# Performance work log

Measured on AMD Instinct MI355X. Metric: run time of the kernel, lower is better.

## Reference

```python
import jax, jax.numpy as jnp
import numpy as np

B, N, D = 4, 8192, 1024
H, DK = 8, 128          # d_k = D // H
FF = 4096
EPS = 1e-5


def setup_inputs() -> dict:
    key = jax.random.key(0)
    ks = jax.random.split(key, 8)
    s = 0.02  # init scale for weights
    return {
        "x": jax.random.normal(ks[0], (B, N, D), jnp.float32),
        "delta_x": jax.random.uniform(ks[1], (N,), jnp.float32),
        # Linear weights stored [in, out] (math-equivalent to torch's x @ W.T)
        "Wq": jax.random.normal(ks[2], (D, D), jnp.float32) * s,
        "bq": jnp.zeros((D,), jnp.float32),
        "Wk": jax.random.normal(ks[3], (D, D), jnp.float32) * s,
        "bk": jnp.zeros((D,), jnp.float32),
        "Wv": jax.random.normal(ks[4], (D, D), jnp.float32) * s,
        "bv": jnp.zeros((D,), jnp.float32),
        # per-head LayerNorm params for K; NOTE: the original code (faithfully
        # reproduced) applies layernorms_K to BOTH key and value in Galerkin mode.
        "gamma_k": jnp.ones((H, DK), jnp.float32),
        "beta_k": jnp.zeros((H, DK), jnp.float32),
        "W1": jax.random.normal(ks[5], (D, FF), jnp.float32) * s,
        "b1": jnp.zeros((FF,), jnp.float32),
        "W2": jax.random.normal(ks[6], (FF, D), jnp.float32) * s,
        "b2": jnp.zeros((D,), jnp.float32),
    }


def _per_head_ln(t, gamma, beta):
    # t: [B, H, N, DK]; torch LayerNorm: biased variance over last dim
    mu = jnp.mean(t, axis=-1, keepdims=True)
    var = jnp.mean(jnp.square(t - mu), axis=-1, keepdims=True)
    t = (t - mu) * jax.lax.rsqrt(var + EPS)
    return t * gamma[None, :, None, :] + beta[None, :, None, :]


def reference(x, delta_x, Wq, bq, Wk, bk, Wv, bv, gamma_k, beta_k, W1, b1, W2, b2):
    b, n, d = x.shape

    def heads(y):  # [b, n, d] -> [b, H, n, DK]
        return y.reshape(b, n, H, DK).transpose(0, 2, 1, 3)

    q = heads(x @ Wq + bq)
    k = heads(x @ Wk + bk)
    v = heads(x @ Wv + bv)

    k = _per_head_ln(k, gamma_k, beta_k)
    v = _per_head_ln(v, gamma_k, beta_k)  # layernorms_K reused on value (as in source)
    k = k * delta_x[None, None, :, None]  # einsum('bhxd,x->bhxd')

    # Galerkin (softmax-free, linear) attention: (K^T V) / N then Q @ (.)
    scores = jnp.einsum("bhnd,bhne->bhde", k, v) / n  # [b,H,DK,DK]
    attn_out = jnp.einsum("bhnd,bhde->bhne", q, scores)  # [b,H,n,DK]
    # (F.dropout in the source treated as identity: inference/eval semantics)

    x = x + attn_out.transpose(0, 2, 1, 3).reshape(b, n, d)  # residual 1
    h = jax.nn.silu(x @ W1 + b1)
    return x + (h @ W2 + b2)  # residual 2
```

## Files before the change

### kernel.cpp

```cpp
#include <hip/hip_runtime.h>
#include <hip/hip_bf16.h>
#include <stdint.h>

#define DEV __device__ __forceinline__

typedef __attribute__((ext_vector_type(8))) short bf16x8;
typedef __attribute__((ext_vector_type(8))) unsigned short u16x8;
typedef __attribute__((ext_vector_type(4))) unsigned short u16x4;
typedef __attribute__((ext_vector_type(4))) float f32x4;

static constexpr int BB = 4, NN = 8192, DD = 1024, HH = 8, DKK = 128, FFF = 4096;
static constexpr int MM = BB * NN;

DEV float bfb2f(unsigned int s) { unsigned int x = s << 16; float f; __builtin_memcpy(&f, &x, 4); return f; }
DEV unsigned short f2bfb(float f) {
    unsigned int x; __builtin_memcpy(&x, &f, 4);
    x += 0x7fffu + ((x >> 16) & 1u);
    return (unsigned short)(x >> 16);
}

DEV void gload_lds16(const void* g, void* l) {
    auto gp = (const __attribute__((address_space(1))) void*)(uintptr_t)g;
    auto lp = (__attribute__((address_space(3))) void*)(unsigned int)(uintptr_t)l;
    __builtin_amdgcn_global_load_lds(gp, lp, 16, 0, 0);
}

__global__ void k_pack_bf16(const float* __restrict__ in, unsigned short* __restrict__ ob, long n) {
    long i = ((long)blockIdx.x * blockDim.x + threadIdx.x) * 8;
    if (i >= n) return;
    f32x4 a = *(const f32x4*)&in[i];
    f32x4 b = *(const f32x4*)&in[i + 4];
    u16x8 o;
    o[0]=f2bfb(a[0]); o[1]=f2bfb(a[1]); o[2]=f2bfb(a[2]); o[3]=f2bfb(a[3]);
    o[4]=f2bfb(b[0]); o[5]=f2bfb(b[1]); o[6]=f2bfb(b[2]); o[7]=f2bfb(b[3]);
    *(u16x8*)&ob[i] = o;
}

__global__ void k_transpose(const float* __restrict__ W, unsigned short* __restrict__ WT, int R, int C) {
    __shared__ float t[32][33];
    const int tid = threadIdx.x;
    const int r0 = blockIdx.y * 32, c0 = blockIdx.x * 32;
    const int lr = tid >> 3, lc = (tid & 7) * 4;
    f32x4 v = *(const f32x4*)&W[(long)(r0 + lr) * C + c0 + lc];
    t[lr][lc + 0] = v[0]; t[lr][lc + 1] = v[1]; t[lr][lc + 2] = v[2]; t[lr][lc + 3] = v[3];
    __syncthreads();
    const int oc = tid >> 3, orr = (tid & 7) * 4;
    u16x4 o;
    o[0] = f2bfb(t[orr + 0][oc]); o[1] = f2bfb(t[orr + 1][oc]);
    o[2] = f2bfb(t[orr + 2][oc]); o[3] = f2bfb(t[orr + 3][oc]);
    *(u16x4*)&WT[(long)(c0 + oc) * R + r0 + orr] = o;
}

template <int EPI>
__global__ __launch_bounds__(512, 2)
void k_gemm256(const unsigned short* __restrict__ A, int lda,
               const unsigned short* __restrict__ BT, int ldbt,
               const float* __restrict__ bias0, const float* __restrict__ bias1,
               const float* __restrict__ bias2,
               const unsigned short* __restrict__ resb,
               unsigned short* __restrict__ outp0, unsigned short* __restrict__ outp1,
               unsigned short* __restrict__ outp2,
               float* __restrict__ outf,
               int K, int gridx)
{
    extern __shared__ __align__(128) unsigned short smem[];
    unsigned short* As = smem;
    unsigned short* Bs = smem + 4 * 8192;

    const int nwg = gridDim.x;
    int wg = blockIdx.x;
    {
        const int q = nwg >> 3, r = nwg & 7;
        const int xcd = wg & 7, idx = wg >> 3;
        wg = (xcd < r ? xcd * (q + 1) : r * (q + 1) + (xcd - r) * q) + idx;
    }
    const int brow = (wg / gridx) * 256;
    const int bcol = (wg % gridx) * 256;

    const int tid = threadIdx.x;
    const int lane = tid & 63;
    const int w = tid >> 6;
    const int wm = w >> 2, wn = w & 3;
    const int fr = lane & 15;
    const int kg = lane >> 4;

    const int dl = tid * 16;
    const int soff = dl ^ (((dl >> 7) & 3) << 4);
    const int arow = soff >> 6;
    const int akel = (soff & 63) >> 1;
    const unsigned short* Abase = A + (long)(brow + arow) * lda + akel;
    const unsigned short* Bbase = BT + (long)(bcol + arow) * ldbt + akel;

#define STAGE2(gb, ldg, slot) do { \
        gload_lds16((gb), (slot) + tid * 8); \
        gload_lds16((gb) + 128 * (long)(ldg), (slot) + 4096 + tid * 8); } while (0)

    auto lds_frag = [&](const unsigned short* slot, int row) -> bf16x8 {
        int off = row * 64 + kg * 16;
        off ^= ((off >> 7) & 3) << 4;
        return *(const bf16x8*)((const char*)slot + off);
    };

    f32x4 acc[8][4] = {};

    STAGE2(Abase, lda, As);
    STAGE2(Bbase, ldbt, Bs);
    STAGE2(Abase + 32, lda, As + 8192);
    STAGE2(Bbase + 32, ldbt, Bs + 8192);
    asm volatile("s_waitcnt vmcnt(4)" ::: "memory");
    __builtin_amdgcn_s_barrier();

    const int NT = K >> 6;
    for (int t = 0; t < NT; ++t) {
        const unsigned short* a0 = As + ((2 * t) & 3) * 8192;
        const unsigned short* a1 = As + ((2 * t + 1) & 3) * 8192;
        const unsigned short* b0 = Bs + ((2 * t) & 3) * 8192;
        const unsigned short* b1 = Bs + ((2 * t + 1) & 3) * 8192;
        unsigned short* nA0 = As + ((2 * t + 2) & 3) * 8192;
        unsigned short* nA1 = As + ((2 * t + 3) & 3) * 8192;
        unsigned short* nB0 = Bs + ((2 * t + 2) & 3) * 8192;
        unsigned short* nB1 = Bs + ((2 * t + 3) & 3) * 8192;
        const bool st = (t + 1 < NT);
        const long kn = (long)(t + 1) * 64;

        bf16x8 b0f[4], a0f[4], a1f[4], b1f[4], a2f[4], a3f[4];
        if (st) STAGE2(Abase + kn, lda, nA0);
        #pragma unroll
        for (int n = 0; n < 4; ++n) b0f[n] = lds_frag(b0, wn * 64 + n * 16 + fr);
        #pragma unroll
        for (int m = 0; m < 4; ++m) a0f[m] = lds_frag(a0, wm * 128 + m * 16 + fr);
        __builtin_amdgcn_s_setprio(1);
        #pragma unroll
        for (int m = 0; m < 4; ++m)
            #pragma unroll
            for (int n = 0; n < 4; ++n)
                acc[m][n] = __builtin_amdgcn_mfma_f32_16x16x32_bf16(a0f[m], b0f[n], acc[m][n], 0, 0, 0);
        __builtin_amdgcn_s_setprio(0);
        __builtin_amdgcn_s_barrier();
        if (st) STAGE2(Bbase + kn, ldbt, nB0);
        #pragma unroll
        for (int m = 0; m < 4; ++m) a1f[m] = lds_frag(a0, wm * 128 + (m + 4) * 16 + fr);
        __builtin_amdgcn_s_setprio(1);
        #pragma unroll
        for (int m = 0; m < 4; ++m)
            #pragma unroll
            for (int n = 0; n < 4; ++n)
                acc[m + 4][n] = __builtin_amdgcn_mfma_f32_16x16x32_bf16(a1f[m], b0f[n], acc[m + 4][n], 0, 0, 0);
        __builtin_amdgcn_s_setprio(0);
        asm volatile("s_waitcnt vmcnt(4)" ::: "memory");
        __builtin_amdgcn_s_barrier();
        if (st) STAGE2(Abase + kn + 32, lda, nA1);
        #pragma unroll
        for (int n = 0; n < 4; ++n) b1f[n] = lds_frag(b1, wn * 64 + n * 16 + fr);
        #pragma unroll
        for (int m = 0; m < 4; ++m) a2f[m] = lds_frag(a1, wm * 128 + m * 16 + fr);
        __builtin_amdgcn_s_setprio(1);
        #pragma unroll
        for (int m = 0; m < 4; ++m)
            #pragma unroll
            for (int n = 0; n < 4; ++n)
                acc[m][n] = __builtin_amdgcn_mfma_f32_16x16x32_bf16(a2f[m], b1f[n], acc[m][n], 0, 0, 0);
        __builtin_amdgcn_s_setprio(0);
        __builtin_amdgcn_s_barrier();
        if (st) STAGE2(Bbase + kn + 32, ldbt, nB1);
        #pragma unroll
        for (int m = 0; m < 4; ++m) a3f[m] = lds_frag(a1, wm * 128 + (m + 4) * 16 + fr);
        __builtin_amdgcn_s_setprio(1);
        #pragma unroll
        for (int m = 0; m < 4; ++m)
            #pragma unroll
            for (int n = 0; n < 4; ++n)
                acc[m + 4][n] = __builtin_amdgcn_mfma_f32_16x16x32_bf16(a3f[m], b1f[n], acc[m + 4][n], 0, 0, 0);
        __builtin_amdgcn_s_setprio(0);
        asm volatile("s_waitcnt vmcnt(4)" ::: "memory");
        __builtin_amdgcn_s_barrier();
    }
#undef STAGE2

    const int q4 = (lane >> 4) * 4;
    if constexpr (EPI == 1) {
        const int mat = bcol >> 10;
        const float* bp = mat == 0 ? bias0 : (mat == 1 ? bias1 : bias2);
        unsigned short* op = mat == 0 ? outp0 : (mat == 1 ? outp1 : outp2);
        const int dc0 = bcol & 1023;
        #pragma unroll
        for (int m = 0; m < 8; ++m)
            #pragma unroll
            for (int n = 0; n < 4; ++n) {
                const int c = dc0 + wn * 64 + n * 16 + fr;
                const float bv = bp[c];
                const int hh = c >> 7, dk = c & 127;
                #pragma unroll
                for (int j = 0; j < 4; ++j) {
                    const int r = brow + wm * 128 + m * 16 + q4 + j;
                    const long idx = (((long)(r >> 13) * 8 + hh) * 8192 + (r & 8191)) * 128 + dk;
                    op[idx] = f2bfb(acc[m][n][j] + bv);
                }
            }
    } else if constexpr (EPI == 2) {
        #pragma unroll
        for (int m = 0; m < 8; ++m)
            #pragma unroll
            for (int n = 0; n < 4; ++n) {
                const int c = bcol + wn * 64 + n * 16 + fr;
                const float bv = bias0[c];
                #pragma unroll
                for (int j = 0; j < 4; ++j) {
                    const int r = brow + wm * 128 + m * 16 + q4 + j;
                    float v = acc[m][n][j] + bv;
                    v = v / (1.f + __expf(-v));
                    outp0[(long)r * FFF + c] = f2bfb(v);
                }
            }
    } else {
        #pragma unroll
        for (int m = 0; m < 8; ++m)
            #pragma unroll
            for (int n = 0; n < 4; ++n) {
                const int c = bcol + wn * 64 + n * 16 + fr;
                const float bv = bias0[c];
                #pragma unroll
                for (int j = 0; j < 4; ++j) {
                    const int r = brow + wm * 128 + m * 16 + q4 + j;
                    float v = acc[m][n][j] + bv + bfb2f(resb[(long)r * DD + c]);
                    outf[(long)r * DD + c] = v;
                }
            }
    }
}

template <int EPI>
__global__ __launch_bounds__(256, 2)
void k_gemm(const unsigned short* __restrict__ A, int lda, long sAz,
            const unsigned short* __restrict__ BT, int ldbt, long sBz,
            const float* __restrict__ bias,
            const float* __restrict__ resf,
            const unsigned short* __restrict__ resb,
            unsigned short* __restrict__ outp,
            float* __restrict__ outf,
            int K)
{
    __shared__ __align__(16) unsigned short As[128 * 32];
    __shared__ __align__(16) unsigned short Bs[128 * 32];
    const int tid = threadIdx.x;
    const int z = blockIdx.z;
    A  += (long)z * sAz;
    BT += (long)z * sBz;
    const int brow = blockIdx.y * 128;
    const int bcol = blockIdx.x * 128;

    const int c0 = tid, c1 = tid + 256;
    const unsigned short* Ap0 = A + (long)(brow + (c0 >> 2)) * lda + (c0 & 3) * 8;
    const unsigned short* Ap1 = A + (long)(brow + (c1 >> 2)) * lda + (c1 & 3) * 8;
    const unsigned short* Bp0 = BT + (long)(bcol + (c0 >> 2)) * ldbt + (c0 & 3) * 8;
    const unsigned short* Bp1 = BT + (long)(bcol + (c1 >> 2)) * ldbt + (c1 & 3) * 8;
    unsigned short* AsD0 = &As[c0 * 8];
    unsigned short* AsD1 = &As[c1 * 8];
    unsigned short* BsD0 = &Bs[c0 * 8];
    unsigned short* BsD1 = &Bs[c1 * 8];

    const int lane = tid & 63;
    const int w = tid >> 6;
    const int wr = (w >> 1) * 64;
    const int wc = (w & 1) * 64;
    const int fr = lane & 15;
    const int fk = (lane >> 4) * 8;

    f32x4 acc[4][4] = {};

    for (int kt = 0; kt < K; kt += 32) {
        gload_lds16(Ap0 + kt, AsD0);
        gload_lds16(Ap1 + kt, AsD1);
        gload_lds16(Bp0 + kt, BsD0);
        gload_lds16(Bp1 + kt, BsD1);
        __syncthreads();
        bf16x8 af[4], bfr[4];
        #pragma unroll
        for (int m = 0; m < 4; ++m) af[m] = *(const bf16x8*)&As[(wr + m * 16 + fr) * 32 + fk];
        #pragma unroll
        for (int n = 0; n < 4; ++n) bfr[n] = *(const bf16x8*)&Bs[(wc + n * 16 + fr) * 32 + fk];
        #pragma unroll
        for (int m = 0; m < 4; ++m)
            #pragma unroll
            for (int n = 0; n < 4; ++n)
                acc[m][n] = __builtin_amdgcn_mfma_f32_16x16x32_bf16(af[m], bfr[n], acc[m][n], 0, 0, 0);
        __syncthreads();
    }

    const int orow = (lane >> 4) * 4;
    #pragma unroll
    for (int m = 0; m < 4; ++m) {
        #pragma unroll
        for (int n = 0; n < 4; ++n) {
            const int d = bcol + wc + n * 16 + fr;
            #pragma unroll
            for (int j = 0; j < 4; ++j) {
                const int r = brow + wr + m * 16 + orow + j;
                float v = acc[m][n][j];
                if constexpr (EPI == 3) {
                    long xi = ((long)(z >> 3) * NN + r) * DD + (z & 7) * DKK + d;
                    v += resf[xi];
                    outp[xi] = f2bfb(v);
                }
            }
        }
    }
    (void)bias; (void)resb; (void)outf;
}

__global__ void k_ln(unsigned short* __restrict__ Kb, unsigned short* __restrict__ Vb,
                     const float* __restrict__ gk, const float* __restrict__ bek,
                     const float* __restrict__ dx)
{
    const int tid = threadIdx.x;
    const int lane = tid & 63;
    const long row = (long)blockIdx.x * 4 + (tid >> 6);
    unsigned short* buf = blockIdx.y ? Vb : Kb;
    const int h = (int)((row >> 13) & 7);
    const int n = (int)(row & 8191);
    unsigned int* p = (unsigned int*)(buf + row * 128) + lane;
    const unsigned int u = *p;
    float f0 = bfb2f(u & 0xffffu);
    float f1 = bfb2f(u >> 16);
    float s = f0 + f1, q = f0 * f0 + f1 * f1;
    #pragma unroll
    for (int o = 32; o; o >>= 1) { s += __shfl_xor(s, o); q += __shfl_xor(q, o); }
    const float mean = s * (1.f / 128.f);
    const float var  = q * (1.f / 128.f) - mean * mean;
    const float rstd = rsqrtf(var + 1e-5f);
    const int gi = h * 128 + lane * 2;
    float o0 = (f0 - mean) * rstd * gk[gi]     + bek[gi];
    float o1 = (f1 - mean) * rstd * gk[gi + 1] + bek[gi + 1];
    if (blockIdx.y == 0) { const float dl = dx[n]; o0 *= dl; o1 *= dl; }
    *p = (unsigned int)f2bfb(o0) | ((unsigned int)f2bfb(o1) << 16);
}

__global__ __launch_bounds__(256, 2)
void k_scorespart(const unsigned short* __restrict__ Kb, const unsigned short* __restrict__ Vb,
                  float* __restrict__ part)
{
    __shared__ __align__(16) unsigned short KT[128 * 136];
    __shared__ __align__(16) unsigned short VT[128 * 136];
    const int tid = threadIdx.x;
    const int bh = blockIdx.y, split = blockIdx.x;
    const unsigned short* Kp = Kb + (long)bh * NN * DKK;
    const unsigned short* Vp = Vb + (long)bh * NN * DKK;
    const int lane = tid & 63, w = tid >> 6;
    const int wr = (w >> 1) * 64, wc = (w & 1) * 64, fr = lane & 15, fk = (lane >> 4) * 8;
    const int nrow = tid >> 1, dblk = (tid & 1) * 64;
    f32x4 acc[4][4] = {};
    for (int c = 0; c < 8; ++c) {
        const int n0 = (split * 8 + c) * 128;
        bf16x8 kv[8], vv[8];
        #pragma unroll
        for (int i = 0; i < 8; ++i) {
            kv[i] = *(const bf16x8*)&Kp[(long)(n0 + nrow) * DKK + dblk + i * 8];
            vv[i] = *(const bf16x8*)&Vp[(long)(n0 + nrow) * DKK + dblk + i * 8];
        }
        __syncthreads();
        #pragma unroll
        for (int i = 0; i < 8; ++i)
            #pragma unroll
            for (int j = 0; j < 8; ++j) {
                const int dd = dblk + i * 8 + j;
                KT[dd * 136 + nrow] = (unsigned short)kv[i][j];
                VT[dd * 136 + nrow] = (unsigned short)vv[i][j];
            }
        __syncthreads();
        #pragma unroll
        for (int ks = 0; ks < 4; ++ks) {
            bf16x8 af[4], bfr[4];
            #pragma unroll
            for (int m = 0; m < 4; ++m) af[m] = *(const bf16x8*)&KT[(wr + m * 16 + fr) * 136 + ks * 32 + fk];
            #pragma unroll
            for (int n = 0; n < 4; ++n) bfr[n] = *(const bf16x8*)&VT[(wc + n * 16 + fr) * 136 + ks * 32 + fk];
            #pragma unroll
            for (int m = 0; m < 4; ++m)
                #pragma unroll
                for (int n = 0; n < 4; ++n)
                    acc[m][n] = __builtin_amdgcn_mfma_f32_16x16x32_bf16(af[m], bfr[n], acc[m][n], 0, 0, 0);
        }
    }
    float* P = part + (long)(bh * 8 + split) * 16384;
    const int orow = (lane >> 4) * 4;
    #pragma unroll
    for (int m = 0; m < 4; ++m)
        #pragma unroll
        for (int n = 0; n < 4; ++n)
            #pragma unroll
            for (int j = 0; j < 4; ++j) {
                const int dD = wr + m * 16 + orow + j;
                const int e  = wc + n * 16 + fr;
                P[dD * 128 + e] = acc[m][n][j];
            }
}

__global__ void k_scoresred(const float* __restrict__ part, unsigned short* __restrict__ scT)
{
    const int bh = blockIdx.x, tid = threadIdx.x;
    const float* P = part + (long)bh * 8 * 16384;
    for (int i = tid; i < 16384; i += 256) {
        float s = 0.f;
        #pragma unroll
        for (int sp = 0; sp < 8; ++sp) s += P[sp * 16384 + i];
        const int d = i >> 7, e = i & 127;
        scT[(long)bh * 16384 + e * 128 + d] = f2bfb(s * (1.f / 8192.f));
    }
}

extern "C" void kernel_launch(void* const* d_in, const int* in_sizes, int n_in,
                              void* d_out, int out_size, void* d_ws, size_t ws_size,
                              hipStream_t stream)
{
    const float* x   = (const float*)d_in[0];
    const float* dx  = (const float*)d_in[1];
    const float* Wq  = (const float*)d_in[2];
    const float* bq  = (const float*)d_in[3];
    const float* Wk  = (const float*)d_in[4];
    const float* bk  = (const float*)d_in[5];
    const float* Wv  = (const float*)d_in[6];
    const float* bv  = (const float*)d_in[7];
    const float* gk  = (const float*)d_in[8];
    const float* bek = (const float*)d_in[9];
    const float* W1  = (const float*)d_in[10];
    const float* b1  = (const float*)d_in[11];
    const float* W2  = (const float*)d_in[12];
    const float* b2  = (const float*)d_in[13];
    float* out = (float*)d_out;
    (void)in_sizes; (void)n_in; (void)out_size; (void)ws_size;

    hipFuncSetAttribute((const void*)k_gemm256<1>, hipFuncAttributeMaxDynamicSharedMemorySize, 131072);
    hipFuncSetAttribute((const void*)k_gemm256<2>, hipFuncAttributeMaxDynamicSharedMemorySize, 131072);
    hipFuncSetAttribute((const void*)k_gemm256<3>, hipFuncAttributeMaxDynamicSharedMemorySize, 131072);

    char* ws = (char*)d_ws;
    size_t off = 0;
    auto alloc = [&](size_t bytes) { void* p = ws + off; off += (bytes + 255) & ~(size_t)255; return p; };
    unsigned short* WqkvT = (unsigned short*)alloc((size_t)3 * DD * DD * 2);
    unsigned short* W1T   = (unsigned short*)alloc((size_t)FFF * DD * 2);
    unsigned short* W2T   = (unsigned short*)alloc((size_t)DD * FFF * 2);
    unsigned short* scT   = (unsigned short*)alloc((size_t)32 * 16384 * 2);
    unsigned short* xb    = (unsigned short*)alloc((size_t)MM * DD * 2);
    unsigned short* Kb    = (unsigned short*)alloc((size_t)MM * DD * 2);
    unsigned short* Vb    = (unsigned short*)alloc((size_t)MM * DD * 2);
    unsigned short* x1b   = (unsigned short*)alloc((size_t)MM * DD * 2);
    unsigned short* hb    = xb;
    float* part           = (float*)x1b;
    unsigned short* Qb    = (unsigned short*)out;

    k_pack_bf16<<<dim3(((long)MM * DD) / 8 / 256), 256, 0, stream>>>(x, xb, (long)MM * DD);
    k_transpose<<<dim3(DD / 32, DD / 32), 256, 0, stream>>>(Wq, WqkvT, DD, DD);
    k_transpose<<<dim3(DD / 32, DD / 32), 256, 0, stream>>>(Wk, WqkvT + (size_t)DD * DD, DD, DD);
    k_transpose<<<dim3(DD / 32, DD / 32), 256, 0, stream>>>(Wv, WqkvT + (size_t)2 * DD * DD, DD, DD);
    k_transpose<<<dim3(FFF / 32, DD / 32), 256, 0, stream>>>(W1, W1T, DD, FFF);
    k_transpose<<<dim3(DD / 32, FFF / 32), 256, 0, stream>>>(W2, W2T, FFF, DD);

    k_gemm256<1><<<dim3((MM / 256) * (3072 / 256)), 512, 131072, stream>>>(
        xb, DD, WqkvT, DD, bq, bk, bv, nullptr, Qb, Kb, Vb, nullptr, DD, 3072 / 256);

    k_ln<<<dim3((BB * HH * NN) / 4, 2), 256, 0, stream>>>(Kb, Vb, gk, bek, dx);

    k_scorespart<<<dim3(8, 32), 256, 0, stream>>>(Kb, Vb, part);
    k_scoresred<<<dim3(32), 256, 0, stream>>>(part, scT);

    k_gemm<3><<<dim3(1, NN / 128, BB * HH), 256, 0, stream>>>(Qb, DKK, (long)NN * DKK, scT, DKK, 16384L,
                                                              nullptr, x, nullptr, x1b, nullptr, DKK);

    for (int c = 0; c < 2; ++c) {
        const unsigned short* xc = x1b + (size_t)c * 16384 * DD;
        k_gemm256<2><<<dim3((16384 / 256) * (FFF / 256)), 512, 131072, stream>>>(
            xc, DD, W1T, DD, b1, nullptr, nullptr, nullptr, hb, nullptr, nullptr, nullptr, DD, FFF / 256);
        k_gemm256<3><<<dim3((16384 / 256) * (DD / 256)), 512, 131072, stream>>>(
            hb, FFF, W2T, FFF, b2, nullptr, nullptr, xc, nullptr, nullptr, nullptr,
            out + (size_t)c * 16384 * DD, FFF, DD / 256);
    }
}
```

Before: 1.073 ms.

## Restructure GEMM main loop with unrolled double-tile schedule and precomputed LDS offsets

Rewrites the bf16 MFMA GEMM main loop so two K-tiles are processed per iteration with fixed LDS slot pointers, removing per-iteration modular slot arithmetic. LDS fragment offsets with swizzle are precomputed into registers once. Adds explicit lgkmcnt waits and sched_barriers before each MFMA block and issues global->LDS prefetches after fragment reads. The prefetch is now unconditional; on the last tiles it loads tile 0 again as dummy work. This assumes NT is even and adds extra barriers per iteration.

```diff
diff --git a/kernel.cpp b/kernel.cpp
--- a/kernel.cpp
+++ b/kernel.cpp
@@ -88,94 +88,96 @@
     const int soff = dl ^ (((dl >> 7) & 3) << 4);
     const int arow = soff >> 6;
     const int akel = (soff & 63) >> 1;
-    const unsigned short* Abase = A + (long)(brow + arow) * lda + akel;
-    const unsigned short* Bbase = BT + (long)(bcol + arow) * ldbt + akel;
-
-#define STAGE2(gb, ldg, slot) do { \
-        gload_lds16((gb), (slot) + tid * 8); \
-        gload_lds16((gb) + 128 * (long)(ldg), (slot) + 4096 + tid * 8); } while (0)
-
-    auto lds_frag = [&](const unsigned short* slot, int row) -> bf16x8 {
-        int off = row * 64 + kg * 16;
-        off ^= ((off >> 7) & 3) << 4;
-        return *(const bf16x8*)((const char*)slot + off);
-    };
+    const unsigned short* Ab = A + (long)(brow + arow) * lda + akel;
+    const unsigned short* Bb = BT + (long)(bcol + arow) * ldbt + akel;
+
+    int aoff[8], boff[4];
+    #pragma unroll
+    for (int m = 0; m < 8; ++m) { int o = (wm * 128 + m * 16 + fr) * 64 + kg * 16; aoff[m] = o ^ (((o >> 7) & 3) << 4); }
+    #pragma unroll
+    for (int n = 0; n < 4; ++n) { int o = (wn * 64 + n * 16 + fr) * 64 + kg * 16; boff[n] = o ^ (((o >> 7) & 3) << 4); }
 
     f32x4 acc[8][4] = {};
 
-    STAGE2(Abase, lda, As);
-    STAGE2(Bbase, ldbt, Bs);
-    STAGE2(Abase + 32, lda, As + 8192);
-    STAGE2(Bbase + 32, ldbt, Bs + 8192);
+#define STG_A(u, ks, slot) do { \
+        const unsigned short* _g = Ab + (long)(u) * 64 + (ks) * 32; \
+        gload_lds16(_g,              (slot) + tid * 8); \
+        gload_lds16(_g + 128L * lda, (slot) + 4096 + tid * 8); } while (0)
+#define STG_B(u, ks, slot) do { \
+        const unsigned short* _g = Bb + (long)(u) * 64 + (ks) * 32; \
+        gload_lds16(_g,               (slot) + tid * 8); \
+        gload_lds16(_g + 128L * ldbt, (slot) + 4096 + tid * 8); } while (0)
+
+#define FENCE_MFMA() \
+        __builtin_amdgcn_s_barrier(); \
+        asm volatile("s_waitcnt lgkmcnt(0)" ::: "memory"); \
+        __builtin_amdgcn_sched_barrier(0)
+
+#define MFMA16(AF, BF, R0) \
+        __builtin_amdgcn_s_setprio(1); \
+        _Pragma("unroll") \
+        for (int m = 0; m < 4; ++m) { \
+            _Pragma("unroll") \
+            for (int n = 0; n < 4; ++n) \
+                acc[(R0) + m][n] = __builtin_amdgcn_mfma_f32_16x16x32_bf16(AF[m], BF[n], acc[(R0) + m][n], 0, 0, 0); \
+        } \
+        __builtin_amdgcn_s_setprio(0); \
+        __builtin_amdgcn_s_barrier()
+
+#define DO_TILE(sa0, sa1, sb0, sb1, na0, na1, nb0, nb1, u) do { \
+        bf16x8 b0f[4], b1f[4], af[4]; \
+         \
+        _Pragma("unroll") \
+        for (int n = 0; n < 4; ++n) b0f[n] = *(const bf16x8*)((const char*)(sb0) + boff[n]); \
+        _Pragma("unroll") \
+        for (int m = 0; m < 4; ++m) af[m] = *(const bf16x8*)((const char*)(sa0) + aoff[m]); \
+        STG_A(u, 0, na0); \
+        FENCE_MFMA(); \
+        MFMA16(af, b0f, 0); \
+         \
+        _Pragma("unroll") \
+        for (int m = 0; m < 4; ++m) af[m] = *(const bf16x8*)((const char*)(sa0) + aoff[m + 4]); \
+        STG_B(u, 0, nb0); \
+        asm volatile("s_waitcnt vmcnt(4)" ::: "memory"); \
+        FENCE_MFMA(); \
+        MFMA16(af, b0f, 4); \
+         \
+        _Pragma("unroll") \
+        for (int n = 0; n < 4; ++n) b1f[n] = *(const bf16x8*)((const char*)(sb1) + boff[n]); \
+        _Pragma("unroll") \
+        for (int m = 0; m < 4; ++m) af[m] = *(const bf16x8*)((const char*)(sa1) + aoff[m]); \
+        STG_A(u, 1, na1); \
+        FENCE_MFMA(); \
+        MFMA16(af, b1f, 0); \
+         \
+        _Pragma("unroll") \
+        for (int m = 0; m < 4; ++m) af[m] = *(const bf16x8*)((const char*)(sa1) + aoff[m + 4]); \
+        STG_B(u, 1, nb1); \
+        asm volatile("s_waitcnt vmcnt(4)" ::: "memory"); \
+        FENCE_MFMA(); \
+        MFMA16(af, b1f, 4); \
+    } while (0)
+
+    unsigned short* A0 = As;            unsigned short* A1 = As + 8192;
+    unsigned short* A2 = As + 16384;    unsigned short* A3 = As + 24576;
+    unsigned short* B0 = Bs;            unsigned short* B1 = Bs + 8192;
+    unsigned short* B2 = Bs + 16384;    unsigned short* B3 = Bs + 24576;
+
+    const int NT = K >> 6;
+    STG_A(0, 0, A0); STG_B(0, 0, B0); STG_A(0, 1, A1); STG_B(0, 1, B1);
     asm volatile("s_waitcnt vmcnt(4)" ::: "memory");
     __builtin_amdgcn_s_barrier();
 
-    const int NT = K >> 6;
-    for (int t = 0; t < NT; ++t) {
-        const unsigned short* a0 = As + ((2 * t) & 3) * 8192;
-        const unsigned short* a1 = As + ((2 * t + 1) & 3) * 8192;
-        const unsigned short* b0 = Bs + ((2 * t) & 3) * 8192;
-        const unsigned short* b1 = Bs + ((2 * t + 1) & 3) * 8192;
-        unsigned short* nA0 = As + ((2 * t + 2) & 3) * 8192;
-        unsigned short* nA1 = As + ((2 * t + 3) & 3) * 8192;
-        unsigned short* nB0 = Bs + ((2 * t + 2) & 3) * 8192;
-        unsigned short* nB1 = Bs + ((2 * t + 3) & 3) * 8192;
-        const bool st = (t + 1 < NT);
-        const long kn = (long)(t + 1) * 64;
-
-        bf16x8 b0f[4], a0f[4], a1f[4], b1f[4], a2f[4], a3f[4];
-        if (st) STAGE2(Abase + kn, lda, nA0);
-        #pragma unroll
-        for (int n = 0; n < 4; ++n) b0f[n] = lds_frag(b0, wn * 64 + n * 16 + fr);
-        #pragma unroll
-        for (int m = 0; m < 4; ++m) a0f[m] = lds_frag(a0, wm * 128 + m * 16 + fr);
-        __builtin_amdgcn_s_setprio(1);
-        #pragma unroll
-        for (int m = 0; m < 4; ++m)
-            #pragma unroll
-            for (int n = 0; n < 4; ++n)
-                acc[m][n] = __builtin_amdgcn_mfma_f32_16x16x32_bf16(a0f[m], b0f[n], acc[m][n], 0, 0, 0);
-        __builtin_amdgcn_s_setprio(0);
-        __builtin_amdgcn_s_barrier();
-        if (st) STAGE2(Bbase + kn, ldbt, nB0);
-        #pragma unroll
-        for (int m = 0; m < 4; ++m) a1f[m] = lds_frag(a0, wm * 128 + (m + 4) * 16 + fr);
-        __builtin_amdgcn_s_setprio(1);
-        #pragma unroll
-        for (int m = 0; m < 4; ++m)
-            #pragma unroll
-            for (int n = 0; n < 4; ++n)
-                acc[m + 4][n] = __builtin_amdgcn_mfma_f32_16x16x32_bf16(a1f[m], b0f[n], acc[m + 4][n], 0, 0, 0);
-        __builtin_amdgcn_s_setprio(0);
-        asm volatile("s_waitcnt vmcnt(4)" ::: "memory");
-        __builtin_amdgcn_s_barrier();
-        if (st) STAGE2(Abase + kn + 32, lda, nA1);
-        #pragma unroll
-        for (int n = 0; n < 4; ++n) b1f[n] = lds_frag(b1, wn * 64 + n * 16 + fr);
-        #pragma unroll
-        for (int m = 0; m < 4; ++m) a2f[m] = lds_frag(a1, wm * 128 + m * 16 + fr);
-        __builtin_amdgcn_s_setprio(1);
-        #pragma unroll
-        for (int m = 0; m < 4; ++m)
-            #pragma unroll
-            for (int n = 0; n < 4; ++n)
-                acc[m][n] = __builtin_amdgcn_mfma_f32_16x16x32_bf16(a2f[m], b1f[n], acc[m][n], 0, 0, 0);
-        __builtin_amdgcn_s_setprio(0);
-        __builtin_amdgcn_s_barrier();
-        if (st) STAGE2(Bbase + kn + 32, ldbt, nB1);
-        #pragma unroll
-        for (int m = 0; m < 4; ++m) a3f[m] = lds_frag(a1, wm * 128 + (m + 4) * 16 + fr);
-        __builtin_amdgcn_s_setprio(1);
-        #pragma unroll
-        for (int m = 0; m < 4; ++m)
-            #pragma unroll
-            for (int n = 0; n < 4; ++n)
-                acc[m + 4][n] = __builtin_amdgcn_mfma_f32_16x16x32_bf16(a3f[m], b1f[n], acc[m + 4][n], 0, 0, 0);
-        __builtin_amdgcn_s_setprio(0);
-        asm volatile("s_waitcnt vmcnt(4)" ::: "memory");
-        __builtin_amdgcn_s_barrier();
-    }
-#undef STAGE2
+    for (int t = 0; t < NT; t += 2) {
+        const int u2 = (t + 2 < NT) ? (t + 2) : 0;
+        DO_TILE(A0, A1, B0, B1, A2, A3, B2, B3, t + 1);
+        DO_TILE(A2, A3, B2, B3, A0, A1, B0, B1, u2);
+    }
+#undef DO_TILE
+#undef MFMA16
+#undef FENCE_MFMA
+#undef STG_A
+#undef STG_B
 
     const int q4 = (lane >> 4) * 4;
     if constexpr (EPI == 1) {
```

After: 1.033 ms. -3.7%, faster.
